# Performance work log

Measured on AMD Instinct MI355X. Metric: run time of the kernel, lower is better.

## Reference

```python
import math
import jax, jax.numpy as jnp
import numpy as np

B, H, V, DEPTH = 8, 1024, 32000, 14
LN_EPS = 1e-5


def _structure(depth):
    """Replicates recurse()/expand() index bookkeeping. Pure python, static.
    Returns per-level boolean masks (len 2K, interleaved left/right per parent),
    B_l/B_r of the root, and sibling pair list S, in the exact original order."""
    def rec(idx_start, n, lengths):
        K = len(lengths)
        idxs = list(range(idx_start, idx_start + K))
        B_l = [[i] for i in idxs]
        B_r = [[i] for i in idxs]
        if n > 1:
            pmask = [(L - 1) > 0 for L in lengths]
            mask, child_lengths = [], []
            for L, m in zip(lengths, pmask):
                mask += [m, m]
                if m:
                    child_lengths += [math.ceil((L - 1) ** 0.75), L - 1]
            masks_below, lB_l, lB_r, S = rec(idxs[-1] + 1, n - 1, child_lengths)
            masks = [np.array(mask, dtype=bool)] + masks_below
            j = 0
            for i in range(K):
                if pmask[i]:
                    B_l[i].extend(lB_l[j])
                    B_r[i].extend(lB_r[j + 1])
                    for v_i in lB_r[j]:
                        for v_j in lB_l[j + 1]:
                            S.append((v_i, v_j))
                    j += 2
        else:
            masks, S = [], []
        return masks, B_l, B_r, S

    masks, B_l, B_r, S = rec(0, depth, [depth])
    return masks, B_l[0], B_r[0], S


def setup_inputs() -> dict:
    key = jax.random.key(0)
    ks = jax.random.split(key, 8)
    s = 0.02  # weight scale for numerical sanity
    return {
        'x': jax.random.normal(ks[0], (B, H), jnp.float32),
        'W_in': jax.random.normal(ks[1], (H, H), jnp.float32) * s,
        'b_in': jnp.zeros((H,), jnp.float32),
        'W_g': jax.random.normal(ks[2], (H, H), jnp.float32) * s,
        'b_g': jnp.zeros((H,), jnp.float32),
        'W_cell': jax.random.normal(ks[3], (2 * H, 2 * H), jnp.float32) * s,
        'b_cell': jnp.zeros((2 * H,), jnp.float32),
        'ln_g': jnp.ones((H,), jnp.float32),
        'ln_b': jnp.zeros((H,), jnp.float32),
        'W_leaf': jax.random.normal(ks[4], (H, 2), jnp.float32) * s,
        'b_leaf': jnp.zeros((2,), jnp.float32),
        'W_out': jax.random.normal(ks[5], (H, V), jnp.float32) * s,
        'b_out': jnp.zeros((V,), jnp.float32),
        'depth': DEPTH,
    }


def _layernorm(z, g, b):
    mu = z.mean(-1, keepdims=True)
    var = ((z - mu) ** 2).mean(-1, keepdims=True)
    return (z - mu) * jax.lax.rsqrt(var + LN_EPS) * g + b


def reference(x, W_in, b_in, W_g, b_g, W_cell, b_cell, ln_g, ln_b,
              W_leaf, b_leaf, W_out, b_out, depth):
    masks, Bl0, Br0, S = _structure(int(depth))
    h_dim = x.shape[-1]

    g = x @ W_g + b_g                                     # global_transform, [B,H]
    prev_h = (x @ W_in + b_in)[None]                      # init_parent, [1,B,H]
    prev_ll = jax.nn.log_softmax(prev_h @ W_leaf + b_leaf, axis=-1)  # [1,B,2]

    hs, ls = [prev_h], [prev_ll]
    for mask in masks:                                    # depth-1 static levels
        K, Bb = prev_h.shape[0], prev_h.shape[1]
        inp = jnp.concatenate([prev_h, jnp.broadcast_to(g, prev_h.shape)], axis=-1)
        z = (inp @ W_cell + b_cell).reshape(K, Bb, 2, h_dim)
        branches = jnp.tanh(_layernorm(z, ln_g, ln_b))    # cell: two child states
        log_leaf = jax.nn.log_softmax(branches @ W_leaf + b_leaf, axis=-1)
        ltl = 0.5 * prev_ll[:, :, None, 1:] + log_leaf    # update_logbreak
        fb = branches.transpose(0, 2, 1, 3).reshape(2 * K, Bb, h_dim)  # flatten_struct
        fl = ltl.transpose(0, 2, 1, 3).reshape(2 * K, Bb, 2)
        sel = np.nonzero(mask)[0]                         # static gather indices
        prev_h, prev_ll = fb[sel], fl[sel]
        hs.append(prev_h)
        ls.append(prev_ll)

    hiddens = jnp.concatenate(hs, axis=0)                 # [T,B,H]
    leaves = jnp.concatenate(ls, axis=0)                  # [T,B,2]
    log_words = jax.nn.log_softmax(hiddens @ W_out + b_out, axis=-1)  # [T,B,V]

    start_idxs = jnp.asarray(np.array(Bl0, dtype=np.int32))
    end_idxs = jnp.asarray(np.array(Br0, dtype=np.int32))
    Sarr = np.array(S, dtype=np.int32).reshape(-1, 2)
    out_idxs = jnp.asarray(Sarr[:, 0])
    in_idxs = jnp.asarray(Sarr[:, 1])
    return log_words, leaves, start_idxs, end_idxs, out_idxs, in_idxs
```

## Files before the change

### kernel.cpp

```cpp
#include <hip/hip_runtime.h>
#include <cstdint>
#include <cstddef>


typedef __attribute__((ext_vector_type(4))) float   f4;
typedef __attribute__((ext_vector_type(4))) float   f32x4;
typedef __attribute__((ext_vector_type(8))) __bf16  bf16x8;
typedef __attribute__((ext_vector_type(4))) unsigned short us4;
typedef __attribute__((ext_vector_type(8))) unsigned short us8;

constexpr int DEPTH = 14;
constexpr int Bb = 8;
constexpr int Hd = 1024;
constexpr int Vv = 32000;
constexpr int NT = Vv / 128;
constexpr int MAXT = 512;
constexpr int MAXS = 4096;
constexpr int MAXP = 32;
constexpr float L2E = 1.44269504088896340736f;

struct SB {
  int lvlOff[DEPTH + 1];
  int lvlK[DEPTH];
  int len[MAXT];
  int lch[MAXT], rch[MAXT];
  int parCnt[DEPTH];
  int parRows[DEPTH][MAXP];
  int T;
  int nS;
  int sOut[MAXS], sIn[MAXS];
  int nStart, nEnd;
  int startIdx[16], endIdx[16];
};

constexpr int ceil75(int L) {
  constexpr int t[14] = {0, 1, 2, 3, 3, 4, 4, 5, 5, 6, 6, 7, 7, 7};
  return t[L];
}

constexpr SB build() {
  SB s{};
  for (int i = 0; i < MAXT; i++) { s.lch[i] = -1; s.rch[i] = -1; }
  s.lvlOff[0] = 0; s.lvlK[0] = 1; s.len[0] = DEPTH;
  for (int l = 0; l < DEPTH - 1; l++) {
    int off = s.lvlOff[l], K = s.lvlK[l];
    int nxt = off + K, cnt = 0;
    for (int i = 0; i < K; i++) {
      int g = off + i;
      if (s.len[g] > 1) {
        int gl = nxt + 2 * cnt, gr = gl + 1;
        s.lch[g] = gl; s.rch[g] = gr;
        s.len[gl] = ceil75(s.len[g] - 1);
        s.len[gr] = s.len[g] - 1;
        s.parRows[l][cnt] = g;
        cnt++;
      }
    }
    s.parCnt[l] = cnt;
    s.lvlOff[l + 1] = nxt;
    s.lvlK[l + 1] = 2 * cnt;
  }
  s.T = s.lvlOff[DEPTH - 1] + s.lvlK[DEPTH - 1];
  s.nS = 0;
  for (int l = DEPTH - 2; l >= 0; l--) {
    for (int pi = 0; pi < s.parCnt[l]; pi++) {
      int g = s.parRows[l][pi];
      for (int u = s.lch[g]; u != -1; u = s.rch[u])
        for (int v = s.rch[g]; v != -1; v = s.lch[v]) {
          s.sOut[s.nS] = u; s.sIn[s.nS] = v; s.nS++;
        }
    }
  }
  s.nStart = 0;
  for (int u = 0; u != -1; u = s.lch[u]) s.startIdx[s.nStart++] = u;
  s.nEnd = 0;
  for (int u = 0; u != -1; u = s.rch[u]) s.endIdx[s.nEnd++] = u;
  return s;
}

constexpr SB HS = build();
__device__ const SB DS = build();

struct PR { int v[MAXP]; };

__device__ __forceinline__ unsigned short f2bf(float f) {
  union { float f; unsigned u; } v; v.f = f;
  unsigned r = v.u + 0x7fffu + ((v.u >> 16) & 1u);
  return (unsigned short)(r >> 16);
}

__global__ void k_wout_t(const float* __restrict__ Wout,
                         unsigned short* __restrict__ Wt) {
  __shared__ float t[64][129];
  int tid = threadIdx.x;
  int n0 = blockIdx.x * 128, k0 = blockIdx.y * 64;
#pragma unroll
  for (int i = 0; i < 8; i++) {
    int k = (tid >> 5) + 8 * i;
    int c = (tid & 31) * 4;
    f4 v = *(const f4*)&Wout[(size_t)(k0 + k) * Vv + n0 + c];
    t[k][c] = v.x; t[k][c + 1] = v.y; t[k][c + 2] = v.z; t[k][c + 3] = v.w;
  }
  __syncthreads();
#pragma unroll
  for (int pass = 0; pass < 4; pass++) {
    int n = (tid >> 3) + 32 * pass;
    int ks = (tid & 7) * 8;
    us8 o;
#pragma unroll
    for (int q = 0; q < 8; q++) o[q] = f2bf(t[ks + q][n]);
    *(us8*)&Wt[(size_t)(n0 + n) * Hd + k0 + ks] = o;
  }
}

__global__ void k_wct(const float* __restrict__ Wc,
                      unsigned short* __restrict__ Wct) {
  __shared__ float t[32][33];
  int tx = threadIdx.x, ty = threadIdx.y;
  int n0 = blockIdx.x * 32, k0 = blockIdx.y * 32;
  for (int i = 0; i < 4; i++)
    t[ty + 8 * i][tx] = Wc[(size_t)(k0 + ty + 8 * i) * 2048 + n0 + tx];
  __syncthreads();
  for (int i = 0; i < 4; i++)
    Wct[(size_t)(n0 + ty + 8 * i) * Hd + k0 + tx] = f2bf(t[tx][ty + 8 * i]);
}

__global__ void k_init(const float* __restrict__ x, const float* __restrict__ Wg,
                       const float* __restrict__ bg, const float* __restrict__ Win,
                       const float* __restrict__ bin, float* __restrict__ gbuf,
                       float* __restrict__ hidd, unsigned short* __restrict__ hiddb) {
  __shared__ float xs[Bb * Hd];
  __shared__ float part[Bb][128];
  int tid = threadIdx.x;
  int mat = blockIdx.y;
  const float* W = mat ? Win : Wg;
  const float* bias = mat ? bin : bg;
  for (int i = tid; i < Bb * Hd; i += 256) xs[i] = x[i];
  __syncthreads();
  int c = tid & 127, kh = tid >> 7;
  int col = blockIdx.x * 128 + c;
  float acc[Bb];
#pragma unroll
  for (int b = 0; b < Bb; b++) acc[b] = 0.f;
  for (int k = kh * 512; k < kh * 512 + 512; k++) {
    float w = W[(size_t)k * Hd + col];
#pragma unroll
    for (int b = 0; b < Bb; b++) acc[b] += xs[b * Hd + k] * w;
  }
  if (kh == 1)
    for (int b = 0; b < Bb; b++) part[b][c] = acc[b];
  __syncthreads();
  if (kh == 0) {
    for (int b = 0; b < Bb; b++) {
      float v = acc[b] + part[b][c] + bias[col];
      if (mat == 0) gbuf[b * Hd + col] = v;
      else { hidd[(size_t)b * Hd + col] = v; hiddb[(size_t)b * Hd + col] = f2bf(v); }
    }
  }
}

__global__ void k_gw(const float* __restrict__ gbuf, const float* __restrict__ Wc,
                     const float* __restrict__ bc, float* __restrict__ gW) {
  __shared__ float xs[Bb * Hd];
  __shared__ float part[Bb][128];
  int tid = threadIdx.x;
  for (int i = tid; i < Bb * Hd; i += 256) xs[i] = gbuf[i];
  __syncthreads();
  int c = tid & 127, kh = tid >> 7;
  int col = blockIdx.x * 128 + c;
  float acc[Bb];
#pragma unroll
  for (int b = 0; b < Bb; b++) acc[b] = 0.f;
  for (int k = kh * 512; k < kh * 512 + 512; k++) {
    float w = Wc[(size_t)(Hd + k) * 2048 + col];
#pragma unroll
    for (int b = 0; b < Bb; b++) acc[b] += xs[b * Hd + k] * w;
  }
  if (kh == 1)
    for (int b = 0; b < Bb; b++) part[b][c] = acc[b];
  __syncthreads();
  if (kh == 0)
    for (int b = 0; b < Bb; b++)
      gW[(size_t)b * 2048 + col] = acc[b] + part[b][c] + bc[col];
}

__global__ void k_leaf0(const float* __restrict__ hidd, const float* __restrict__ Wl,
                        const float* __restrict__ bl, float* __restrict__ leaves) {
  int b = threadIdx.x >> 6, lane = threadIdx.x & 63;
  float d0 = 0.f, d1 = 0.f;
  for (int k = lane; k < Hd; k += 64) {
    float h = hidd[(size_t)b * Hd + k];
    d0 += h * Wl[2 * k];
    d1 += h * Wl[2 * k + 1];
  }
  for (int off = 32; off; off >>= 1) {
    d0 += __shfl_down(d0, off);
    d1 += __shfl_down(d1, off);
  }
  if (lane == 0) {
    float l0 = d0 + bl[0], l1 = d1 + bl[1];
    float m = fmaxf(l0, l1);
    float L = logf(expf(l0 - m) + expf(l1 - m));
    leaves[b * 2 + 0] = l0 - m - L;
    leaves[b * 2 + 1] = l1 - m - L;
  }
}

__global__ __launch_bounds__(256) void k_cellg(
    const unsigned short* __restrict__ A, const unsigned short* __restrict__ Bt,
    float* __restrict__ zbuf, PR pr, int Mtot) {
  __shared__ short As[128 * 64];
  __shared__ short Bs[128 * 64];
  int tid = threadIdx.x;
  int lane = tid & 63, w = tid >> 6;
  int wm = w & 1, wn = w >> 1;
  int R0 = blockIdx.x * 128, C0 = blockIdx.y * 128;
  int ks = blockIdx.z;
  f32x4 acc[4][4];
#pragma unroll
  for (int i = 0; i < 4; i++)
#pragma unroll
    for (int j = 0; j < 4; j++) acc[i][j] = 0.f;
  int quad = lane >> 4, l15 = lane & 15;
  int srow = lane >> 3;
  int kc = lane & 7;
  for (int kb = ks * 4; kb < ks * 4 + 4; kb++) {
    int k0 = kb * 64;
#pragma unroll
    for (int i = 0; i < 4; i++) {
      int rowb = w * 32 + i * 8;
      int m = rowb + srow;
      int kcx = kc ^ (m & 7);
      int gr = R0 + m;
      int grc = gr < Mtot ? gr : 0;
      int arow = pr.v[grc >> 3] * Bb + (grc & 7);
      const unsigned short* ga = A + (size_t)arow * Hd + k0 + kcx * 8;
      const unsigned short* gb = Bt + (size_t)(C0 + m) * Hd + k0 + kcx * 8;
      __builtin_amdgcn_global_load_lds(
          (__attribute__((address_space(1))) void*)ga,
          (__attribute__((address_space(3))) void*)&As[rowb * 64], 16, 0, 0);
      __builtin_amdgcn_global_load_lds(
          (__attribute__((address_space(1))) void*)gb,
          (__attribute__((address_space(3))) void*)&Bs[rowb * 64], 16, 0, 0);
    }
    __syncthreads();
#pragma unroll
    for (int ksi = 0; ksi < 2; ksi++) {
      bf16x8 af[4], bfr[4];
      int kidx = ksi * 4 + quad;
#pragma unroll
      for (int i = 0; i < 4; i++) {
        int m = wm * 64 + i * 16 + l15;
        af[i] = *(const bf16x8*)&As[m * 64 + (kidx ^ (m & 7)) * 8];
      }
#pragma unroll
      for (int j = 0; j < 4; j++) {
        int n = wn * 64 + j * 16 + l15;
        bfr[j] = *(const bf16x8*)&Bs[n * 64 + (kidx ^ (n & 7)) * 8];
      }
#pragma unroll
      for (int i = 0; i < 4; i++)
#pragma unroll
        for (int j = 0; j < 4; j++)
          acc[i][j] = __builtin_amdgcn_mfma_f32_16x16x32_bf16(af[i], bfr[j],
                                                              acc[i][j], 0, 0, 0);
    }
    __syncthreads();
  }
#pragma unroll
  for (int j = 0; j < 4; j++) {
    int col = C0 + wn * 64 + j * 16 + l15;
#pragma unroll
    for (int i = 0; i < 4; i++) {
      int rowb = R0 + wm * 64 + i * 16 + quad * 4;
#pragma unroll
      for (int r = 0; r < 4; r++) {
        int row = rowb + r;
        if (row < Mtot)
          zbuf[((size_t)ks * 256 + row) * 2048 + col] = acc[i][j][r];
      }
    }
  }
}

__global__ void k_ln2(const float* __restrict__ zbuf, const float* __restrict__ gW,
                      const float* __restrict__ lng, const float* __restrict__ lnb,
                      const float* __restrict__ Wl, const float* __restrict__ bl,
                      unsigned short* __restrict__ hiddb,
                      float* __restrict__ leaves, PR pr, int lvlOff) {
  __shared__ float a1[4], a2[4], c1[4], c2[4];
  int tid = threadIdx.x, lane = tid & 63, wid = tid >> 6;
  int node = blockIdx.x, b = blockIdx.y;
  int cg = node & 1, p = node >> 1;
  int gp = pr.v[p];
  int ch = lvlOff + node;
  int m = p * Bb + b;
  int j0 = tid * 4;
  size_t zb = (size_t)m * 2048 + cg * 1024 + j0;
  f4 z = *(const f4*)&zbuf[zb];
  z += *(const f4*)&zbuf[zb + (size_t)256 * 2048];
  z += *(const f4*)&zbuf[zb + (size_t)512 * 2048];
  z += *(const f4*)&zbuf[zb + (size_t)768 * 2048];
  z += *(const f4*)&gW[(size_t)b * 2048 + cg * 1024 + j0];
  float s = z.x + z.y + z.z + z.w;
  float s2 = z.x * z.x + z.y * z.y + z.z * z.z + z.w * z.w;
#pragma unroll
  for (int off = 32; off; off >>= 1) {
    s += __shfl_xor(s, off);
    s2 += __shfl_xor(s2, off);
  }
  if (lane == 0) { a1[wid] = s; a2[wid] = s2; }
  __syncthreads();
  s = a1[0] + a1[1] + a1[2] + a1[3];
  s2 = a2[0] + a2[1] + a2[2] + a2[3];
  float mu = s * (1.f / 1024.f);
  float var = s2 * (1.f / 1024.f) - mu * mu;
  float rs = rsqrtf(var + 1e-5f);
  f4 lgv = *(const f4*)&lng[j0];
  f4 lbv = *(const f4*)&lnb[j0];
  f4 y;
  y.x = tanhf((z.x - mu) * rs * lgv.x + lbv.x);
  y.y = tanhf((z.y - mu) * rs * lgv.y + lbv.y);
  y.z = tanhf((z.z - mu) * rs * lgv.z + lbv.z);
  y.w = tanhf((z.w - mu) * rs * lgv.w + lbv.w);
  us4 yb;
  yb.x = f2bf(y.x); yb.y = f2bf(y.y); yb.z = f2bf(y.z); yb.w = f2bf(y.w);
  *(us4*)&hiddb[((size_t)ch * Bb + b) * Hd + j0] = yb;
  f4 wA = *(const f4*)&Wl[j0 * 2];
  f4 wB = *(const f4*)&Wl[j0 * 2 + 4];
  float d0 = y.x * wA.x + y.y * wA.z + y.z * wB.x + y.w * wB.z;
  float d1 = y.x * wA.y + y.y * wA.w + y.z * wB.y + y.w * wB.w;
#pragma unroll
  for (int off = 32; off; off >>= 1) {
    d0 += __shfl_xor(d0, off);
    d1 += __shfl_xor(d1, off);
  }
  if (lane == 0) { c1[wid] = d0; c2[wid] = d1; }
  __syncthreads();
  if (tid == 0) {
    float l0 = c1[0] + c1[1] + c1[2] + c1[3] + bl[0];
    float l1 = c2[0] + c2[1] + c2[2] + c2[3] + bl[1];
    float mm = fmaxf(l0, l1);
    float L = logf(expf(l0 - mm) + expf(l1 - mm));
    float half = 0.5f * leaves[((size_t)gp * Bb + b) * 2 + 1];
    leaves[((size_t)ch * Bb + b) * 2 + 0] = half + l0 - mm - L;
    leaves[((size_t)ch * Bb + b) * 2 + 1] = half + l1 - mm - L;
  }
}

__global__ __launch_bounds__(256) void k_gemm(
    const unsigned short* __restrict__ A, const unsigned short* __restrict__ Bt,
    const float* __restrict__ bout, float* __restrict__ out,
    float2* __restrict__ ptile, int Mvalid) {
  __shared__ short As[128 * 64];
  __shared__ short Bs[128 * 64];
  int tid = threadIdx.x;
  int lane = tid & 63, w = tid >> 6;
  int wm = w & 1, wn = w >> 1;
  int R0 = blockIdx.x * 128, C0 = blockIdx.y * 128;
  f32x4 acc[4][4];
#pragma unroll
  for (int i = 0; i < 4; i++)
#pragma unroll
    for (int j = 0; j < 4; j++) acc[i][j] = 0.f;
  int quad = lane >> 4, l15 = lane & 15;
  int srow = lane >> 3;
  int kc = lane & 7;
  for (int kb = 0; kb < 16; kb++) {
    int k0 = kb * 64;
#pragma unroll
    for (int i = 0; i < 4; i++) {
      int rowb = w * 32 + i * 8;
      int m = rowb + srow;
      int kcx = kc ^ (m & 7);
      const unsigned short* ga = A + (size_t)(R0 + m) * Hd + k0 + kcx * 8;
      const unsigned short* gb = Bt + (size_t)(C0 + m) * Hd + k0 + kcx * 8;
      __builtin_amdgcn_global_load_lds(
          (__attribute__((address_space(1))) void*)ga,
          (__attribute__((address_space(3))) void*)&As[rowb * 64], 16, 0, 0);
      __builtin_amdgcn_global_load_lds(
          (__attribute__((address_space(1))) void*)gb,
          (__attribute__((address_space(3))) void*)&Bs[rowb * 64], 16, 0, 0);
    }
    __syncthreads();
#pragma unroll
    for (int ksi = 0; ksi < 2; ksi++) {
      bf16x8 af[4], bfr[4];
      int kidx = ksi * 4 + quad;
#pragma unroll
      for (int i = 0; i < 4; i++) {
        int m = wm * 64 + i * 16 + l15;
        af[i] = *(const bf16x8*)&As[m * 64 + (kidx ^ (m & 7)) * 8];
      }
#pragma unroll
      for (int j = 0; j < 4; j++) {
        int n = wn * 64 + j * 16 + l15;
        bfr[j] = *(const bf16x8*)&Bs[n * 64 + (kidx ^ (n & 7)) * 8];
      }
#pragma unroll
      for (int i = 0; i < 4; i++)
#pragma unroll
        for (int j = 0; j < 4; j++)
          acc[i][j] = __builtin_amdgcn_mfma_f32_16x16x32_bf16(af[i], bfr[j],
                                                              acc[i][j], 0, 0, 0);
    }
    __syncthreads();
  }
  float2* sred = (float2*)As;
  float bo[4];
#pragma unroll
  for (int j = 0; j < 4; j++) bo[j] = bout[C0 + wn * 64 + j * 16 + l15];
#pragma unroll
  for (int i = 0; i < 4; i++) {
#pragma unroll
    for (int r = 0; r < 4; r++) {
      int lr = wm * 64 + i * 16 + quad * 4 + r;
      int row = R0 + lr;
      float v0 = acc[i][0][r] + bo[0];
      float v1 = acc[i][1][r] + bo[1];
      float v2 = acc[i][2][r] + bo[2];
      float v3 = acc[i][3][r] + bo[3];
      if (row < Mvalid) {
        size_t base = (size_t)row * Vv + C0 + wn * 64 + l15;
        __builtin_nontemporal_store(v0, &out[base + 0]);
        __builtin_nontemporal_store(v1, &out[base + 16]);
        __builtin_nontemporal_store(v2, &out[base + 32]);
        __builtin_nontemporal_store(v3, &out[base + 48]);
      }
      float mx = fmaxf(fmaxf(v0, v1), fmaxf(v2, v3));
#pragma unroll
      for (int d = 1; d < 16; d <<= 1) mx = fmaxf(mx, __shfl_xor(mx, d));
      float sm = exp2f((v0 - mx) * L2E) + exp2f((v1 - mx) * L2E) +
                 exp2f((v2 - mx) * L2E) + exp2f((v3 - mx) * L2E);
#pragma unroll
      for (int d = 1; d < 16; d <<= 1) sm += __shfl_xor(sm, d);
      if (l15 == 0) { sred[wn * 128 + lr].x = mx; sred[wn * 128 + lr].y = sm; }
    }
  }
  __syncthreads();
  if (tid < 128) {
    float2 a = sred[tid], c = sred[128 + tid];
    float M = fmaxf(a.x, c.x);
    float S = a.y * exp2f((a.x - M) * L2E) + c.y * exp2f((c.x - M) * L2E);
    float2 o; o.x = M; o.y = S;
    ptile[(size_t)(R0 + tid) * NT + blockIdx.y] = o;
  }
}

__global__ void k_lse(const float2* __restrict__ ptile, float* __restrict__ st) {
  __shared__ float ms[256], ss[256];
  int r = blockIdx.x, tid = threadIdx.x;
  float mx = -3e38f, sm = 0.f;
  for (int t = tid; t < NT; t += 256) {
    float2 e = ptile[(size_t)r * NT + t];
    float M = fmaxf(mx, e.x);
    sm = sm * exp2f((mx - M) * L2E) + e.y * exp2f((e.x - M) * L2E);
    mx = M;
  }
  ms[tid] = mx; ss[tid] = sm;
  __syncthreads();
  for (int o = 128; o; o >>= 1) {
    if (tid < o) {
      float m2 = ms[tid + o], s2 = ss[tid + o];
      float M = fmaxf(ms[tid], m2);
      ss[tid] = ss[tid] * exp2f((ms[tid] - M) * L2E) + s2 * exp2f((m2 - M) * L2E);
      ms[tid] = M;
    }
    __syncthreads();
  }
  if (tid == 0) st[r] = ms[0] + logf(ss[0]);
}

__global__ void k_norm(float* __restrict__ out, const float* __restrict__ st) {
  int r = blockIdx.y;
  int i = blockIdx.x * 256 + threadIdx.x;
  if (i < Vv / 4) {
    float sub = st[r];
    f4* p = (f4*)(out + (size_t)r * Vv) + i;
    f4 v = __builtin_nontemporal_load(p);
    v -= sub;
    __builtin_nontemporal_store(v, p);
  }
}

__global__ void k_idx(float* __restrict__ dst) {
  int total = DS.nStart + DS.nEnd + 2 * DS.nS;
  for (int i = threadIdx.x; i < total; i += 256) {
    int v;
    if (i < DS.nStart) v = DS.startIdx[i];
    else if (i < DS.nStart + DS.nEnd) v = DS.endIdx[i - DS.nStart];
    else if (i < DS.nStart + DS.nEnd + DS.nS) v = DS.sOut[i - DS.nStart - DS.nEnd];
    else v = DS.sIn[i - DS.nStart - DS.nEnd - DS.nS];
    dst[i] = (float)v;
  }
}

extern "C" void kernel_launch(void* const* d_in, const int* in_sizes, int n_in,
                              void* d_out, int out_size, void* d_ws, size_t ws_size,
                              hipStream_t stream) {
  (void)in_sizes; (void)n_in; (void)out_size; (void)ws_size;
  const float* x    = (const float*)d_in[0];
  const float* Win  = (const float*)d_in[1];
  const float* bin  = (const float*)d_in[2];
  const float* Wg   = (const float*)d_in[3];
  const float* bg   = (const float*)d_in[4];
  const float* Wc   = (const float*)d_in[5];
  const float* bc   = (const float*)d_in[6];
  const float* lng  = (const float*)d_in[7];
  const float* lnb  = (const float*)d_in[8];
  const float* Wl   = (const float*)d_in[9];
  const float* bl   = (const float*)d_in[10];
  const float* Wout = (const float*)d_in[11];
  const float* bout = (const float*)d_in[12];
  float* out = (float*)d_out;

  constexpr int T = HS.T;
  constexpr int Mrows = T * Bb;
  constexpr int Mt = ((Mrows + 127) / 128) * 128;

  char* ws = (char*)d_ws;
  unsigned short* Wt = (unsigned short*)ws;    ws += (size_t)Vv * Hd * 2;
  unsigned short* Wct = (unsigned short*)ws;   ws += (size_t)2048 * Hd * 2;
  float* hidd = (float*)ws;                    ws += (size_t)Bb * Hd * 4;
  unsigned short* hiddb = (unsigned short*)ws; ws += (size_t)Mt * Hd * 2;
  float* gbuf = (float*)ws;                    ws += (size_t)Bb * Hd * 4;
  float* gW = (float*)ws;                      ws += (size_t)Bb * 2048 * 4;
  float* zbuf = (float*)ws;                    ws += (size_t)4 * 256 * 2048 * 4;
  float2* ptile = (float2*)ws;                 ws += (size_t)Mt * NT * 8;
  float* st = (float*)ws;                      ws += (size_t)Mt * 4;

  float* leaves = out + (size_t)Mrows * Vv;
  float* idxdst = leaves + (size_t)Mrows * 2;

  k_wout_t<<<dim3(Vv / 128, Hd / 64), dim3(256), 0, stream>>>(Wout, Wt);
  k_wct<<<dim3(2048 / 32, Hd / 32), dim3(32, 8), 0, stream>>>(Wc, Wct);
  k_init<<<dim3(8, 2), dim3(256), 0, stream>>>(x, Wg, bg, Win, bin, gbuf, hidd, hiddb);
  k_gw<<<dim3(16), dim3(256), 0, stream>>>(gbuf, Wc, bc, gW);
  k_leaf0<<<dim3(1), dim3(512), 0, stream>>>(hidd, Wl, bl, leaves);

  for (int l = 1; l < DEPTH; l++) {
    int Pc = HS.parCnt[l - 1];
    int Mtot = Pc * Bb;
    int Mtiles = (Mtot + 127) / 128;
    PR pr{};
    for (int i = 0; i < Pc; i++) pr.v[i] = HS.parRows[l - 1][i];
    k_cellg<<<dim3(Mtiles, 16, 4), dim3(256), 0, stream>>>(hiddb, Wct, zbuf, pr, Mtot);
    k_ln2<<<dim3(2 * Pc, Bb), dim3(256), 0, stream>>>(zbuf, gW, lng, lnb, Wl, bl,
                                                      hiddb, leaves, pr,
                                                      HS.lvlOff[l]);
  }

  k_gemm<<<dim3(Mt / 128, Vv / 128), dim3(256), 0, stream>>>(hiddb, Wt, bout, out,
                                                             ptile, Mrows);
  k_lse<<<dim3(Mrows), dim3(256), 0, stream>>>(ptile, st);
  k_norm<<<dim3(32, Mrows), dim3(256), 0, stream>>>(out, st);
  k_idx<<<dim3(1), dim3(256), 0, stream>>>(idxdst);
}
```

Before: 1.135 ms.

## Store bf16 logits to workspace, remap gemm tiles per XCD, widen softmax partials

The output GEMM now writes bias-added logits as bf16 into a workspace buffer when the workspace is large enough. The normalize pass then reads these bf16 values, subtracts the log-sum-exp and writes fp32 output. This halves the intermediate write and read traffic, at the cost of rounding the log-probabilities to bf16 precision. The grid becomes 1D with an XCD-aware tile remap so that blocks sharing B columns land on the same XCD, and the per-row max/sum partials skip the shuffle reduction and are combined through LDS instead.

```diff
diff --git a/kernel.cpp b/kernel.cpp
--- a/kernel.cpp
+++ b/kernel.cpp
@@ -348,16 +348,26 @@
   }
 }
 
+constexpr int MT_TILES = 22;
+constexpr int NWG = MT_TILES * NT;
+
+template <int BF>
 __global__ __launch_bounds__(256) void k_gemm(
     const unsigned short* __restrict__ A, const unsigned short* __restrict__ Bt,
-    const float* __restrict__ bout, float* __restrict__ out,
-    float2* __restrict__ ptile, int Mvalid) {
+    const float* __restrict__ bout, float* __restrict__ outf,
+    unsigned short* __restrict__ lgt, float2* __restrict__ ptile, int Mvalid) {
   __shared__ short As[128 * 64];
   __shared__ short Bs[128 * 64];
   int tid = threadIdx.x;
   int lane = tid & 63, w = tid >> 6;
   int wm = w & 1, wn = w >> 1;
-  int R0 = blockIdx.x * 128, C0 = blockIdx.y * 128;
+  int bid = blockIdx.x;
+  constexpr int q = NWG >> 3, r = NWG & 7;
+  int xcd = bid & 7, idx = bid >> 3;
+  int wgid = (xcd < r ? xcd * (q + 1) : r * (q + 1) + (xcd - r) * q) + idx;
+  int ny = wgid / MT_TILES;
+  int mx = wgid - ny * MT_TILES;
+  int R0 = mx * 128, C0 = ny * 128;
   f32x4 acc[4][4];
 #pragma unroll
   for (int i = 0; i < 4; i++)
@@ -406,44 +416,61 @@
     }
     __syncthreads();
   }
-  float2* sred = (float2*)As;
+  float2* s0 = (float2*)As;
+  float2* s1 = (float2*)Bs;
+  float2* sw = wn ? s1 : s0;
   float bo[4];
 #pragma unroll
   for (int j = 0; j < 4; j++) bo[j] = bout[C0 + wn * 64 + j * 16 + l15];
 #pragma unroll
   for (int i = 0; i < 4; i++) {
 #pragma unroll
-    for (int r = 0; r < 4; r++) {
-      int lr = wm * 64 + i * 16 + quad * 4 + r;
+    for (int r2 = 0; r2 < 4; r2++) {
+      int lr = wm * 64 + i * 16 + quad * 4 + r2;
       int row = R0 + lr;
-      float v0 = acc[i][0][r] + bo[0];
-      float v1 = acc[i][1][r] + bo[1];
-      float v2 = acc[i][2][r] + bo[2];
-      float v3 = acc[i][3][r] + bo[3];
+      float v0 = acc[i][0][r2] + bo[0];
+      float v1 = acc[i][1][r2] + bo[1];
+      float v2 = acc[i][2][r2] + bo[2];
+      float v3 = acc[i][3][r2] + bo[3];
       if (row < Mvalid) {
         size_t base = (size_t)row * Vv + C0 + wn * 64 + l15;
-        __builtin_nontemporal_store(v0, &out[base + 0]);
-        __builtin_nontemporal_store(v1, &out[base + 16]);
-        __builtin_nontemporal_store(v2, &out[base + 32]);
-        __builtin_nontemporal_store(v3, &out[base + 48]);
+        if (BF) {
+          __builtin_nontemporal_store(f2bf(v0), &lgt[base + 0]);
+          __builtin_nontemporal_store(f2bf(v1), &lgt[base + 16]);
+          __builtin_nontemporal_store(f2bf(v2), &lgt[base + 32]);
+          __builtin_nontemporal_store(f2bf(v3), &lgt[base + 48]);
+        } else {
+          __builtin_nontemporal_store(v0, &outf[base + 0]);
+          __builtin_nontemporal_store(v1, &outf[base + 16]);
+          __builtin_nontemporal_store(v2, &outf[base + 32]);
+          __builtin_nontemporal_store(v3, &outf[base + 48]);
+        }
       }
-      float mx = fmaxf(fmaxf(v0, v1), fmaxf(v2, v3));
-#pragma unroll
-      for (int d = 1; d < 16; d <<= 1) mx = fmaxf(mx, __shfl_xor(mx, d));
-      float sm = exp2f((v0 - mx) * L2E) + exp2f((v1 - mx) * L2E) +
-                 exp2f((v2 - mx) * L2E) + exp2f((v3 - mx) * L2E);
-#pragma unroll
-      for (int d = 1; d < 16; d <<= 1) sm += __shfl_xor(sm, d);
-      if (l15 == 0) { sred[wn * 128 + lr].x = mx; sred[wn * 128 + lr].y = sm; }
+      float mx4 = fmaxf(fmaxf(v0, v1), fmaxf(v2, v3));
+      float sm4 = exp2f((v0 - mx4) * L2E) + exp2f((v1 - mx4) * L2E) +
+                  exp2f((v2 - mx4) * L2E) + exp2f((v3 - mx4) * L2E);
+      float2 e; e.x = mx4; e.y = sm4;
+      sw[lr * 16 + l15] = e;
     }
   }
   __syncthreads();
   if (tid < 128) {
-    float2 a = sred[tid], c = sred[128 + tid];
-    float M = fmaxf(a.x, c.x);
-    float S = a.y * exp2f((a.x - M) * L2E) + c.y * exp2f((c.x - M) * L2E);
+    int rot = tid & 15;
+    float M = -3e38f;
+#pragma unroll
+    for (int t = 0; t < 16; t++) {
+      int c = (t + rot) & 15;
+      M = fmaxf(M, fmaxf(s0[tid * 16 + c].x, s1[tid * 16 + c].x));
+    }
+    float S = 0.f;
+#pragma unroll
+    for (int t = 0; t < 16; t++) {
+      int c = (t + rot) & 15;
+      float2 a = s0[tid * 16 + c], b = s1[tid * 16 + c];
+      S += a.y * exp2f((a.x - M) * L2E) + b.y * exp2f((b.x - M) * L2E);
+    }
     float2 o; o.x = M; o.y = S;
-    ptile[(size_t)(R0 + tid) * NT + blockIdx.y] = o;
+    ptile[(size_t)(R0 + tid) * NT + ny] = o;
   }
 }
 
@@ -483,6 +510,32 @@
   }
 }
 
+__global__ void k_norm_bf(const unsigned short* __restrict__ lgt,
+                          float* __restrict__ out, const float* __restrict__ st) {
+  int r = blockIdx.y;
+  int i = blockIdx.x * 256 + threadIdx.x;
+  if (i < Vv / 8) {
+    float sub = st[r];
+    us8 v = __builtin_nontemporal_load((const us8*)(lgt + (size_t)r * Vv + i * 8));
+    f4 o0, o1;
+#pragma unroll
+    for (int qk = 0; qk < 4; qk++) {
+      union { unsigned u; float f; } cv;
+      cv.u = ((unsigned)v[qk]) << 16;
+      o0[qk] = cv.f - sub;
+    }
+#pragma unroll
+    for (int qk = 0; qk < 4; qk++) {
+      union { unsigned u; float f; } cv;
+      cv.u = ((unsigned)v[4 + qk]) << 16;
+      o1[qk] = cv.f - sub;
+    }
+    float* p = out + (size_t)r * Vv + i * 8;
+    __builtin_nontemporal_store(o0, (f4*)p);
+    __builtin_nontemporal_store(o1, (f4*)(p + 4));
+  }
+}
+
 __global__ void k_idx(float* __restrict__ dst) {
   int total = DS.nStart + DS.nEnd + 2 * DS.nS;
   for (int i = threadIdx.x; i < total; i += 256) {
@@ -498,7 +551,7 @@
 extern "C" void kernel_launch(void* const* d_in, const int* in_sizes, int n_in,
                               void* d_out, int out_size, void* d_ws, size_t ws_size,
                               hipStream_t stream) {
-  (void)in_sizes; (void)n_in; (void)out_size; (void)ws_size;
+  (void)in_sizes; (void)n_in; (void)out_size;
   const float* x    = (const float*)d_in[0];
   const float* Win  = (const float*)d_in[1];
   const float* bin  = (const float*)d_in[2];
@@ -519,6 +572,7 @@
   constexpr int Mt = ((Mrows + 127) / 128) * 128;
 
   char* ws = (char*)d_ws;
+  char* ws0 = ws;
   unsigned short* Wt = (unsigned short*)ws;    ws += (size_t)Vv * Hd * 2;
   unsigned short* Wct = (unsigned short*)ws;   ws += (size_t)2048 * Hd * 2;
   float* hidd = (float*)ws;                    ws += (size_t)Bb * Hd * 4;
@@ -528,6 +582,9 @@
   float* zbuf = (float*)ws;                    ws += (size_t)4 * 256 * 2048 * 4;
   float2* ptile = (float2*)ws;                 ws += (size_t)Mt * NT * 8;
   float* st = (float*)ws;                      ws += (size_t)Mt * 4;
+  unsigned short* lgt = (unsigned short*)ws;
+  size_t needBf = (size_t)(ws - ws0) + (size_t)Mt * Vv * 2;
+  bool bfp = ws_size >= needBf;
 
   float* leaves = out + (size_t)Mrows * Vv;
   float* idxdst = leaves + (size_t)Mrows * 2;
@@ -550,9 +607,16 @@
                                                       HS.lvlOff[l]);
   }
 
-  k_gemm<<<dim3(Mt / 128, Vv / 128), dim3(256), 0, stream>>>(hiddb, Wt, bout, out,
-                                                             ptile, Mrows);
-  k_lse<<<dim3(Mrows), dim3(256), 0, stream>>>(ptile, st);
-  k_norm<<<dim3(32, Mrows), dim3(256), 0, stream>>>(out, st);
+  if (bfp) {
+    k_gemm<1><<<dim3(NWG), dim3(256), 0, stream>>>(hiddb, Wt, bout, out, lgt,
+                                                   ptile, Mrows);
+    k_lse<<<dim3(Mrows), dim3(256), 0, stream>>>(ptile, st);
+    k_norm_bf<<<dim3(16, Mrows), dim3(256), 0, stream>>>(lgt, out, st);
+  } else {
+    k_gemm<0><<<dim3(NWG), dim3(256), 0, stream>>>(hiddb, Wt, bout, out, lgt,
+                                                   ptile, Mrows);
+    k_lse<<<dim3(Mrows), dim3(256), 0, stream>>>(ptile, st);
+    k_norm<<<dim3(32, Mrows), dim3(256), 0, stream>>>(out, st);
+  }
   k_idx<<<dim3(1), dim3(256), 0, stream>>>(idxdst);
 }
```

Result: no change. 1.118 ms (-1.5%).
